# Optimization experiments

Hardware: AMD Instinct MI355X
Metric: run time of the kernel (lower is better)

Reference implementation:

```python
import jax, jax.numpy as jnp
import numpy as np

# GPT-2 small structural constants (hardcoded in the original module)
L, H, D, DH, F, V, P, S, NC = 12, 12, 768, 64, 3072, 50257, 1024, 128, 29

def _ln(x, g, b, eps=1e-5):
    m = x.mean(-1, keepdims=True)
    v = ((x - m) ** 2).mean(-1, keepdims=True)
    return (x - m) * jax.lax.rsqrt(v + eps) * g + b

def _split_w(W):  # [D, D] -> [H, D, DH]: torch _split_heads on the last (output) dim
    return jnp.transpose(W.reshape(D, H, DH), (1, 0, 2))

def _attn_heads(xln, Wqh, Wkh, Wvh, Woh, qb, kb, vb, mask):
    # xln: [H, S, D] per-head circuit inputs. Computes the weight-product attention
    # branch: (xln@Wq+bq)(xln@Wk+bk)^T scores (algebraically identical to the four
    # W_mhqk bias-expanded terms in the source), causal softmax, then
    # attn @ ((xln@Wv+bv) @ W_mho) which equals attn@Output_mhov + attn@bv_Wo.
    q = jnp.einsum('hse,hed->hsd', xln, Wqh) + qb[:, None, :]
    k = jnp.einsum('hse,hed->hsd', xln, Wkh) + kb[:, None, :]
    v = jnp.einsum('hse,hed->hsd', xln, Wvh) + vb[:, None, :]
    s = jnp.einsum('hsd,htd->hst', q, k) / (DH ** 0.5)
    s = jnp.where(mask, s, jnp.finfo(s.dtype).min)
    a = jax.nn.softmax(s, axis=-1)
    ctx = jnp.einsum('hst,htd->hsd', a, v)
    return jnp.einsum('hsd,hdf->hsf', ctx, Woh)  # [H, S, D]

def _check1(x, r, records):
    # check_representation: subtract refined-matrix-gated recorded circuit tensors
    # from layers 0..i-1 (rows >= i of records are still zero, so full contraction
    # equals contracting records[0:i+1]).
    return x - jnp.einsum('lc,lcsd->sd', r, records)

def _checkH(x, rh, records):  # batched over the 12 per-head checks
    return x[None] - jnp.einsum('hlc,lcsd->hsd', rh, records)

def _forward(input_ids, refined_matrix, wte, wpe, qkv_w, qkv_b, proj_w, proj_b,
             ln1_g, ln1_b, ln2_g, ln2_b, fc_w, fc_b, mproj_w, mproj_b, lnf_g, lnf_b):
    rm = refined_matrix.astype(wte.dtype)                 # [L*NC, L, NC]
    h = wte[input_ids[0]] + wpe[:S]                       # [S, D]
    records = jnp.zeros((L, NC, S, D), dtype=h.dtype)     # record_circuit_tensor_all
    mask = jnp.tril(jnp.ones((S, S), dtype=bool))
    gelu = lambda x: jax.nn.gelu(x, approximate=True)     # GPT-2 gelu_new
    for i in range(L):
        Wq, Wk, Wv = jnp.split(qkv_w[i], 3, axis=1)
        Wqh, Wkh, Wvh = _split_w(Wq), _split_w(Wk), _split_w(Wv)
        qb = qkv_b[i][:D].reshape(H, DH)
        kb = qkv_b[i][D:2 * D].reshape(H, DH)
        vb = qkv_b[i][2 * D:].reshape(H, DH)
        Woh = proj_w[i].reshape(H, DH, D)                 # W_mho per head
        base = i * NC
        if i > 0:
            c1 = _check1(h, rm[base], records)                       # check 0
            x2 = _checkH(h, rm[base + 1:base + 1 + H], records)      # checks 1..12
            x3 = _check1(h, rm[base + 13], records)                  # check 13
            x4 = _checkH(h, rm[base + 14:base + 14 + H], records)    # checks 14..25
        else:
            c1, x3 = h, h
            x2 = jnp.broadcast_to(h, (H, S, D))
            x4 = x2
        # circuit 2: per-head attention via weight products
        x2ln = _ln(x2, ln1_g[i], ln1_b[i])
        head2 = _attn_heads(x2ln, Wqh, Wkh, Wvh, Woh, qb, kb, vb, mask)
        c2 = head2.sum(0)
        residual = c1 + c2 + proj_b[i]                    # + W_obias
        # full MLP stream on the residual (with c_fc bias, no c_proj bias)
        stream = gelu(_ln(residual, ln2_g[i], ln2_b[i]) @ fc_w[i] + fc_b[i]) @ mproj_w[i]
        # circuit 3: bias-free MLP of the (double-LN'd) checked layer input
        x3ln = _ln(_ln(x3, ln1_g[i], ln1_b[i]), ln2_g[i], ln2_b[i])
        c3 = gelu(x3ln @ fc_w[i]) @ mproj_w[i]
        # circuit 4: per-head attention branch -> MLP composition
        x4ln = _ln(x4, ln1_g[i], ln1_b[i])
        head4 = _attn_heads(x4ln, Wqh, Wkh, Wvh, Woh, qb, kb, vb, mask)
        c4_heads = gelu(_ln(head4, ln2_g[i], ln2_b[i]) @ fc_w[i]) @ mproj_w[i]
        c5 = stream - c3 - c4_heads.sum(0)                # nonlinearity compensation
        c6 = jnp.broadcast_to(mproj_b[i], (S, D))
        ob = jnp.broadcast_to(proj_b[i], (S, D))
        rec = jnp.concatenate([c1[None], head2, c3[None], c4_heads,
                               c5[None], c6[None], ob[None]], axis=0)  # [29, S, D]
        records = records.at[i].set(rec)
        h = residual + stream + mproj_b[i]
    return _ln(h, lnf_g, lnf_b) @ wte.T                   # logits [S, V]

def setup_inputs():
    key = jax.random.key(0)
    ks = jax.random.split(key, 16)
    sd = 0.02
    n = lambda k, shp: (jax.random.normal(k, shp) * sd).astype(jnp.float32)
    return {
        'input_ids': jax.random.randint(ks[0], (1, S), 0, V),
        'label_ids': jax.random.randint(ks[1], (1, S), 0, V),
        'refined_matrix': jax.random.randint(ks[2], (L * NC, L, NC), 0, 2).astype(jnp.int32),
        'wte': n(ks[3], (V, D)),
        'wpe': n(ks[4], (P, D)),
        'qkv_w': n(ks[5], (L, D, 3 * D)),
        'qkv_b': n(ks[6], (L, 3 * D)),
        'proj_w': n(ks[7], (L, D, D)),
        'proj_b': n(ks[8], (L, D)),
        'ln1_g': jnp.ones((L, D), jnp.float32),
        'ln1_b': jnp.zeros((L, D), jnp.float32),
        'ln2_g': jnp.ones((L, D), jnp.float32),
        'ln2_b': jnp.zeros((L, D), jnp.float32),
        'fc_w': n(ks[9], (L, D, F)),
        'fc_b': n(ks[10], (L, F)),
        'mproj_w': n(ks[11], (L, F, D)),
        'mproj_b': n(ks[12], (L, D)),
        'lnf_g': jnp.ones((D,), jnp.float32),
        'lnf_b': jnp.zeros((D,), jnp.float32),
    }

def reference(input_ids, label_ids, refined_matrix, wte, wpe, qkv_w, qkv_b, proj_w, proj_b,
              ln1_g, ln1_b, ln2_g, ln2_b, fc_w, fc_b, mproj_w, mproj_b, lnf_g, lnf_b):
    return _forward(input_ids, refined_matrix, wte, wpe, qkv_w, qkv_b, proj_w, proj_b,
                    ln1_g, ln1_b, ln2_g, ln2_b, fc_w, fc_b, mproj_w, mproj_b, lnf_g, lnf_b)
```

## Files before the change

kernel.cpp:

```cpp
#include <hip/hip_runtime.h>

#define SS 128
#define DD 768
#define HH 12
#define DHD 64
#define FF 3072
#define VV 50257
#define NCC 29
#define LL 12
#define SD (SS*DD)
#define SF (SS*FF)
#define TMAX (LL*NCC)

typedef unsigned short u16;
typedef __attribute__((ext_vector_type(8))) short short8;
typedef __attribute__((ext_vector_type(4))) float f32x4;

__device__ inline u16 f2bf(float f) {
    union { float f; unsigned u; } x; x.f = f;
    unsigned r = x.u + 0x7fffu + ((x.u >> 16) & 1u);
    return (u16)(r >> 16);
}

__global__ void k_masku(const int* __restrict__ rm, unsigned* __restrict__ lmu) {
    int idx = blockIdx.x * 256 + threadIdx.x;
    if (idx >= LL * TMAX) return;
    int i = idx / TMAX, t = idx % TMAX;
    unsigned m = 0;
    for (int j = 0; j < 26; j++)
        m |= (unsigned)(rm[(size_t)(i * NCC + j) * TMAX + t] & 1) << j;
    lmu[idx] = m;
}

__global__ void k_embed(const int* __restrict__ ids, const float* __restrict__ wte,
                        const float* __restrict__ wpe, float* __restrict__ h) {
    int sd = blockIdx.x * 256 + threadIdx.x;
    if (sd >= SD) return;
    int s = sd / DD, d = sd % DD;
    h[sd] = wte[(size_t)ids[s] * DD + d] + wpe[sd];
}

__global__ void k_cvt(const float* __restrict__ in, u16* __restrict__ out, int n4) {
    int i = blockIdx.x * 256 + threadIdx.x;
    if (i >= n4) return;
    float4 v = *(const float4*)(in + (size_t)i * 4);
    u16* o = out + (size_t)i * 4;
    o[0] = f2bf(v.x); o[1] = f2bf(v.y); o[2] = f2bf(v.z); o[3] = f2bf(v.w);
}

__global__ void k_qkvb(const float* __restrict__ qkv_b, float* __restrict__ qkvbp) {
    int idx = blockIdx.x * 256 + threadIdx.x;
    if (idx >= LL * 3 * DD) return;
    int l = idx / (3 * DD), r = idx % (3 * DD);
    int p = r / DD, rem = r % DD, h = rem / DHD, j = rem % DHD;
    qkvbp[(size_t)l * 3 * DD + h * 192 + p * DHD + j] = qkv_b[idx];
}

__global__ __launch_bounds__(256) void k_wt(const float* __restrict__ W, u16* __restrict__ WT,
                                            int K, int N, int remap,
                                            long long sW, long long sWT) {
    __shared__ float T[64][65];
    const float* Wb = W + (size_t)blockIdx.z * sW;
    u16* WTb = WT + (size_t)blockIdx.z * sWT;
    int n0 = blockIdx.x * 64, k0 = blockIdx.y * 64;
    int c = threadIdx.x & 63, r0 = threadIdx.x >> 6;
#pragma unroll
    for (int i = 0; i < 16; i++) {
        int r = r0 + 4 * i;
        T[r][c] = Wb[(size_t)(k0 + r) * N + n0 + c];
    }
    __syncthreads();
    int ob = n0 >> 6;
    if (remap) { int p = ob / 12, h = ob % 12; ob = h * 3 + p; }
    size_t orow0 = (size_t)ob * 64;
#pragma unroll
    for (int i = 0; i < 16; i++) {
        int a = r0 + 4 * i;
        WTb[(orow0 + a) * K + k0 + c] = f2bf(T[c][a]);
    }
}

__global__ __launch_bounds__(256) void k_check(
    const float* __restrict__ records, const unsigned* __restrict__ lmu,
    const float* __restrict__ h, float* __restrict__ rec0, float* __restrict__ x24,
    float* __restrict__ x3, int layer) {
    __shared__ float red[4][26][128];
    int lane = threadIdx.x & 63, w = threadIdx.x >> 6;
    int sd0 = blockIdx.x * 128;
    int sd = sd0 + lane * 2;
    int T = layer * NCC;
    int Tq = (T + 3) >> 2;
    int tb = w * Tq, te = tb + Tq; if (te > T) te = T;
    float2 acc[26];
#pragma unroll
    for (int j = 0; j < 26; j++) { acc[j].x = 0.f; acc[j].y = 0.f; }
    const unsigned* lm = lmu + layer * TMAX;
    const float* rp = records + sd;
    int t = tb;
    for (; t + 8 <= te; t += 8) {
        float2 r[8];
        unsigned mv[8];
#pragma unroll
        for (int u = 0; u < 8; u++) r[u] = *(const float2*)(rp + (size_t)(t + u) * SD);
#pragma unroll
        for (int u = 0; u < 8; u++) mv[u] = lm[t + u];
#pragma unroll
        for (int u = 0; u < 8; u++) {
            unsigned m = __builtin_amdgcn_readfirstlane(mv[u]);
#pragma unroll
            for (int j = 0; j < 26; j++) {
                float mm = (m & (1u << j)) ? 1.0f : 0.0f;
                acc[j].x = fmaf(mm, r[u].x, acc[j].x);
                acc[j].y = fmaf(mm, r[u].y, acc[j].y);
            }
        }
    }
    for (; t < te; t++) {
        float2 r = *(const float2*)(rp + (size_t)t * SD);
        unsigned m = __builtin_amdgcn_readfirstlane(lm[t]);
#pragma unroll
        for (int j = 0; j < 26; j++) {
            float mm = (m & (1u << j)) ? 1.0f : 0.0f;
            acc[j].x = fmaf(mm, r.x, acc[j].x);
            acc[j].y = fmaf(mm, r.y, acc[j].y);
        }
    }
#pragma unroll
    for (int j = 0; j < 26; j++)
        *(float2*)&red[w][j][lane * 2] = acc[j];
    __syncthreads();
    for (int o = threadIdx.x; o < 26 * 128; o += 256) {
        int j = o >> 7, sdl = o & 127;
        float s = red[0][j][sdl] + red[1][j][sdl] + red[2][j][sdl] + red[3][j][sdl];
        float v = h[sd0 + sdl] - s;
        float* dst;
        if (j == 0) dst = rec0;
        else if (j <= 12) dst = x24 + (size_t)(j - 1) * SD;
        else if (j == 13) dst = x3;
        else dst = x24 + (size_t)(12 + j - 14) * SD;
        dst[sd0 + sdl] = v;
    }
}

__device__ inline void wave_ln(float (&vals)[12], int lane, const float* __restrict__ g,
                               const float* __restrict__ b) {
    float s = 0.f;
#pragma unroll
    for (int i = 0; i < 12; i++) s += vals[i];
#pragma unroll
    for (int m = 32; m >= 1; m >>= 1) s += __shfl_xor(s, m, 64);
    float mean = s * (1.f / DD);
    float vs = 0.f;
#pragma unroll
    for (int i = 0; i < 12; i++) { float d = vals[i] - mean; vs += d * d; }
#pragma unroll
    for (int m = 32; m >= 1; m >>= 1) vs += __shfl_xor(vs, m, 64);
    float rstd = rsqrtf(vs * (1.f / DD) + 1e-5f);
#pragma unroll
    for (int i = 0; i < 12; i++)
        vals[i] = (vals[i] - mean) * rstd * g[lane + 64 * i] + b[lane + 64 * i];
}

__global__ __launch_bounds__(256) void k_ln(const float* __restrict__ in, float* __restrict__ outf,
                                            u16* __restrict__ outb,
                                            const float* __restrict__ g, const float* __restrict__ b,
                                            int R) {
    int row = blockIdx.x * 4 + (threadIdx.x >> 6);
    if (row >= R) return;
    int lane = threadIdx.x & 63;
    const float* x = in + (size_t)row * DD;
    float vals[12];
#pragma unroll
    for (int i = 0; i < 12; i++) vals[i] = x[lane + 64 * i];
    wave_ln(vals, lane, g, b);
#pragma unroll
    for (int i = 0; i < 12; i++) {
        int d = lane + 64 * i;
        if (outf) outf[(size_t)row * DD + d] = vals[i];
        if (outb) outb[(size_t)row * DD + d] = f2bf(vals[i]);
    }
}

__global__ __launch_bounds__(256) void k_rln(const float* __restrict__ reci,
                                             const float* __restrict__ x3,
                                             const float* __restrict__ tmp4,
                                             const float* __restrict__ proj_b_i,
                                             float* __restrict__ resid,
                                             u16* __restrict__ mlpAb,
                                             const float* __restrict__ l1g, const float* __restrict__ l1b,
                                             const float* __restrict__ l2g, const float* __restrict__ l2b) {
    int rowid = blockIdx.x * 4 + (threadIdx.x >> 6);
    int z = rowid >> 7, s = rowid & 127;
    int lane = threadIdx.x & 63;
    float vals[12];
    if (z == 0) {
        const float* src = x3 + (size_t)s * DD;
#pragma unroll
        for (int i = 0; i < 12; i++) vals[i] = src[lane + 64 * i];
        wave_ln(vals, lane, l1g, l1b);
    } else if (z <= 12) {
        const float* src = tmp4 + (size_t)(z - 1) * SD + (size_t)s * DD;
#pragma unroll
        for (int i = 0; i < 12; i++) vals[i] = src[lane + 64 * i];
    } else {
        const float* base = reci + (size_t)s * DD;
#pragma unroll
        for (int i = 0; i < 12; i++) {
            int d = lane + 64 * i;
            float a = base[d];
#pragma unroll
            for (int j = 1; j <= 12; j++) a += base[(size_t)j * SD + d];
            a += proj_b_i[d];
            vals[i] = a;
            resid[(size_t)s * DD + d] = a;
        }
    }
    wave_ln(vals, lane, l2g, l2b);
    u16* o = mlpAb + (size_t)z * SD + (size_t)s * DD;
#pragma unroll
    for (int i = 0; i < 12; i++) o[lane + 64 * i] = f2bf(vals[i]);
}

__global__ __launch_bounds__(256) void k_mm(
    const u16* __restrict__ A, const u16* __restrict__ BT,
    const float* __restrict__ bias, void* __restrict__ Cv, void* __restrict__ Cv2,
    int N, int K, int lda, int ldbt, int ldc,
    long long sA, long long sBT, long long sC, long long sBias,
    int zMod, int zHi, int biasLo, int mode) {
    __shared__ u16 As[128][40];
    __shared__ u16 Bs[64][40];
    int z = blockIdx.z;
    int zb = z % zMod;
    const u16* Ab = A + (size_t)z * sA;
    const u16* Bb = BT + (size_t)zb * sBT;
    int n0 = blockIdx.x * 64;
    int nSplit = gridDim.y;
    int kLen = K / nSplit;
    int kOff = blockIdx.y * kLen;
    int kEnd = kOff + kLen;
    int tid = threadIdx.x;
    int lane = tid & 63, wid = tid >> 6;
    int wm = (wid >> 1) * 64, wn = (wid & 1) * 32;
    int l15 = lane & 15, l4 = lane >> 4;
    int sr = tid >> 2, sseg = tid & 3;
    int bn = n0 + sr;
    f32x4 acc[4][2];
#pragma unroll
    for (int i = 0; i < 4; i++) { acc[i][0] = (f32x4)0.f; acc[i][1] = (f32x4)0.f; }
    uint4 zero; zero.x = 0u; zero.y = 0u; zero.z = 0u; zero.w = 0u;
    uint4 a0 = *(const uint4*)(Ab + (size_t)sr * lda + kOff + sseg * 8);
    uint4 a1 = *(const uint4*)(Ab + (size_t)(sr + 64) * lda + kOff + sseg * 8);
    uint4 bv = (bn < N) ? *(const uint4*)(Bb + (size_t)bn * ldbt + kOff + sseg * 8) : zero;
    for (int k0 = kOff; k0 < kEnd; k0 += 32) {
        __syncthreads();
        *(uint4*)&As[sr][sseg * 8] = a0;
        *(uint4*)&As[sr + 64][sseg * 8] = a1;
        *(uint4*)&Bs[sr][sseg * 8] = bv;
        __syncthreads();
        if (k0 + 32 < kEnd) {
            a0 = *(const uint4*)(Ab + (size_t)sr * lda + k0 + 32 + sseg * 8);
            a1 = *(const uint4*)(Ab + (size_t)(sr + 64) * lda + k0 + 32 + sseg * 8);
            bv = (bn < N) ? *(const uint4*)(Bb + (size_t)bn * ldbt + k0 + 32 + sseg * 8) : zero;
        }
        short8 af[4], bfr[2];
#pragma unroll
        for (int i = 0; i < 4; i++) af[i] = *(const short8*)&As[wm + i * 16 + l15][l4 * 8];
#pragma unroll
        for (int j = 0; j < 2; j++) bfr[j] = *(const short8*)&Bs[wn + j * 16 + l15][l4 * 8];
#pragma unroll
        for (int i = 0; i < 4; i++)
#pragma unroll
            for (int j = 0; j < 2; j++)
                acc[i][j] = __builtin_amdgcn_mfma_f32_16x16x32_bf16(af[i], bfr[j], acc[i][j], 0, 0, 0);
    }
    const float* bp = (bias != nullptr && z >= biasLo) ? bias + (size_t)zb * sBias : nullptr;
    void* Cuse;
    int zc;
    if (nSplit > 1) { Cuse = Cv; zc = z * nSplit + blockIdx.y; }
    else { Cuse = (z >= zHi) ? Cv2 : Cv; zc = (z >= zHi) ? z - zHi : z; }
    if (mode == 0) {
        float* Cb = (float*)Cuse + (size_t)zc * sC;
#pragma unroll
        for (int i = 0; i < 4; i++) {
            int row = wm + i * 16 + l4 * 4;
#pragma unroll
            for (int j = 0; j < 2; j++) {
                int col = n0 + wn + j * 16 + l15;
                if (col >= N) continue;
                float bb = bp ? bp[col] : 0.f;
#pragma unroll
                for (int r = 0; r < 4; r++)
                    Cb[(size_t)(row + r) * ldc + col] = acc[i][j][r] + bb;
            }
        }
    } else {
        u16* Cb = (u16*)Cuse + (size_t)zc * sC;
#pragma unroll
        for (int i = 0; i < 4; i++) {
            int row = wm + i * 16 + l4 * 4;
#pragma unroll
            for (int j = 0; j < 2; j++) {
                int col = n0 + wn + j * 16 + l15;
                if (col >= N) continue;
                float bb = bp ? bp[col] : 0.f;
#pragma unroll
                for (int r = 0; r < 4; r++) {
                    float v = acc[i][j][r] + bb;
                    float c = v + 0.044715f * v * v * v;
                    float gv = 0.5f * v * (1.f + tanhf(0.7978845608028654f * c));
                    Cb[(size_t)(row + r) * ldc + col] = f2bf(gv);
                }
            }
        }
    }
}

__global__ __launch_bounds__(256) void k_attn(const float* __restrict__ qkvp,
                                              const float* __restrict__ qbias,
                                              u16* __restrict__ ctx) {
    __shared__ float kv[SS * DHD];
    __shared__ float qs[16][DHD];
    __shared__ float sc[16][130];
    int z = blockIdx.y, s0 = blockIdx.x * 16;
    const float* p0 = qkvp + (size_t)z * 4 * (SS * 192);
    const float* p1 = p0 + SS * 192;
    const float* p2 = p1 + SS * 192;
    const float* p3 = p2 + SS * 192;
    const float* qb = qbias + (size_t)(z % 12) * 192;
    int tid = threadIdx.x;
    for (int idx = tid; idx < SS * DHD; idx += 256) {
        int t = idx >> 6, d = idx & 63;
        int o = t * 192 + 64 + d;
        kv[idx] = p0[o] + p1[o] + p2[o] + p3[o] + qb[64 + d];
    }
    for (int idx = tid; idx < 16 * DHD; idx += 256) {
        int r = idx >> 6, d = idx & 63;
        int o = (s0 + r) * 192 + d;
        qs[r][d] = p0[o] + p1[o] + p2[o] + p3[o] + qb[d];
    }
    __syncthreads();
    int r = tid >> 4, tt = tid & 15;
    int s = s0 + r;
    float pl[8];
#pragma unroll
    for (int u = 0; u < 8; u++) {
        int t = tt + 16 * u;
        float dot;
        if (t <= s) {
            dot = 0.f;
            for (int d = 0; d < DHD; d++) dot += qs[r][d] * kv[t * DHD + d];
            dot *= 0.125f;
        } else {
            dot = -1e30f;
        }
        pl[u] = dot;
    }
    float mx = pl[0];
#pragma unroll
    for (int u = 1; u < 8; u++) mx = fmaxf(mx, pl[u]);
#pragma unroll
    for (int m = 1; m < 16; m <<= 1) mx = fmaxf(mx, __shfl_xor(mx, m, 16));
    float sum = 0.f;
#pragma unroll
    for (int u = 0; u < 8; u++) { pl[u] = __expf(pl[u] - mx); sum += pl[u]; }
#pragma unroll
    for (int m = 1; m < 16; m <<= 1) sum += __shfl_xor(sum, m, 16);
    float inv = 1.f / sum;
#pragma unroll
    for (int u = 0; u < 8; u++) sc[r][tt + 16 * u] = pl[u] * inv;
    __syncthreads();
    for (int idx = tid; idx < SS * DHD; idx += 256) {
        int t = idx >> 6, d = idx & 63;
        int o = t * 192 + 128 + d;
        kv[idx] = p0[o] + p1[o] + p2[o] + p3[o] + qb[128 + d];
    }
    __syncthreads();
    int d = tid & 63, r0 = tid >> 6;
#pragma unroll
    for (int u = 0; u < 4; u++) {
        int rr = r0 + 4 * u;
        float a = 0.f;
        for (int t = 0; t < SS; t++) a += sc[rr][t] * kv[t * DHD + d];
        ctx[(size_t)z * SS * DHD + (size_t)(s0 + rr) * DHD + d] = f2bf(a);
    }
}

__global__ void k_red(const float* __restrict__ part, const float* __restrict__ resid,
                      const float* __restrict__ proj_b_i, const float* __restrict__ mproj_b_i,
                      float* __restrict__ reci, float* __restrict__ h) {
    int sd = blockIdx.x * 256 + threadIdx.x;
    if (sd >= SD) return;
    int d = sd % DD;
    float v0 = 0.f, s4 = 0.f, st = 0.f;
#pragma unroll
    for (int zz = 0; zz < 14; zz++) {
        const float* p = part + (size_t)zz * 4 * SD + sd;
        float v = p[0] + p[SD] + p[2 * SD] + p[3 * SD];
        if (zz == 0) { v0 = v; reci[(size_t)13 * SD + sd] = v; }
        else if (zz <= 12) { s4 += v; reci[(size_t)(13 + zz) * SD + sd] = v; }
        else st = v;
    }
    reci[(size_t)26 * SD + sd] = st - v0 - s4;
    reci[(size_t)27 * SD + sd] = mproj_b_i[d];
    reci[(size_t)28 * SD + sd] = proj_b_i[d];
    h[sd] = resid[sd] + st + mproj_b_i[d];
}

extern "C" void kernel_launch(void* const* d_in, const int* in_sizes, int n_in,
                              void* d_out, int out_size, void* d_ws, size_t ws_size,
                              hipStream_t stream) {
    const int* ids = (const int*)d_in[0];
    const int* rm = (const int*)d_in[2];
    const float* wte = (const float*)d_in[3];
    const float* wpe = (const float*)d_in[4];
    const float* qkv_w = (const float*)d_in[5];
    const float* qkv_b = (const float*)d_in[6];
    const float* proj_w = (const float*)d_in[7];
    const float* proj_b = (const float*)d_in[8];
    const float* ln1_g = (const float*)d_in[9];
    const float* ln1_b = (const float*)d_in[10];
    const float* ln2_g = (const float*)d_in[11];
    const float* ln2_b = (const float*)d_in[12];
    const float* fc_w = (const float*)d_in[13];
    const float* fc_b = (const float*)d_in[14];
    const float* mproj_w = (const float*)d_in[15];
    const float* mproj_b = (const float*)d_in[16];
    const float* lnf_g = (const float*)d_in[17];
    const float* lnf_b = (const float*)d_in[18];
    float* out = (float*)d_out;

    float* ws = (float*)d_ws;
    size_t off = 0;
    float* records = ws + off; off += (size_t)LL * NCC * SD;
    float* x24  = ws + off; off += (size_t)24 * SD;
    float* tmp4 = ws + off; off += (size_t)12 * SD;
    float* h    = ws + off; off += SD;
    float* x3   = ws + off; off += SD;
    float* resid= ws + off; off += SD;
    float* qkvp = ws + off; off += (size_t)24 * 4 * SS * 192;
    float* mpp  = ws + off; off += (size_t)14 * 4 * SD;
    float* qkvbp= ws + off; off += (size_t)LL * 3 * DD;
    u16* xlnb  = (u16*)(ws + off); off += (size_t)24 * SD / 2;
    u16* mlpAb = (u16*)(ws + off); off += (size_t)14 * SD / 2;
    u16* hfcb  = (u16*)(ws + off); off += (size_t)14 * SF / 2;
    u16* ctxb  = (u16*)(ws + off); off += (size_t)24 * SS * DHD / 2;
    u16* lnfb  = (u16*)(ws + off); off += SD / 2;
    u16* qkvhT = (u16*)(ws + off); off += (size_t)LL * 2304 * DD / 2;
    u16* fcT   = (u16*)(ws + off); off += (size_t)LL * FF * DD / 2;
    u16* mprojT= (u16*)(ws + off); off += (size_t)LL * DD * FF / 2;
    u16* projT = (u16*)(ws + off); off += (size_t)LL * DD * DD / 2;
    u16* wteb  = (u16*)(ws + off); off += (size_t)VV * DD / 2;
    unsigned* lmu = (unsigned*)(ws + off);

    k_masku<<<(LL * TMAX + 255) / 256, 256, 0, stream>>>(rm, lmu);
    k_embed<<<SD / 256, 256, 0, stream>>>(ids, wte, wpe, h);
    k_cvt<<<((VV * DD / 4) + 255) / 256, 256, 0, stream>>>(wte, wteb, VV * DD / 4);
    k_qkvb<<<(LL * 3 * DD + 255) / 256, 256, 0, stream>>>(qkv_b, qkvbp);
    k_wt<<<dim3(36, 12, 12), 256, 0, stream>>>(qkv_w, qkvhT, DD, 3 * DD, 1,
                                               (long long)DD * 3 * DD, (long long)2304 * DD);
    k_wt<<<dim3(48, 12, 12), 256, 0, stream>>>(fc_w, fcT, DD, FF, 0,
                                               (long long)DD * FF, (long long)FF * DD);
    k_wt<<<dim3(12, 48, 12), 256, 0, stream>>>(mproj_w, mprojT, FF, DD, 0,
                                               (long long)FF * DD, (long long)DD * FF);
    k_wt<<<dim3(12, 12, 12), 256, 0, stream>>>(proj_w, projT, DD, DD, 0,
                                               (long long)DD * DD, (long long)DD * DD);

    for (int i = 0; i < LL; i++) {
        float* reci = records + (size_t)i * NCC * SD;
        const float* l1g = ln1_g + i * DD; const float* l1b = ln1_b + i * DD;
        const float* l2g = ln2_g + i * DD; const float* l2b = ln2_b + i * DD;
        const u16* qkvhTi = qkvhT + (size_t)i * 2304 * DD;
        const u16* fcTi = fcT + (size_t)i * FF * DD;
        const u16* mprojTi = mprojT + (size_t)i * DD * FF;
        const u16* projTi = projT + (size_t)i * DD * DD;

        k_check<<<SD / 128, 256, 0, stream>>>(records, lmu, h, reci, x24, x3, i);

        k_ln<<<24 * SS / 4, 256, 0, stream>>>(x24, nullptr, xlnb, l1g, l1b, 24 * SS);
        k_mm<<<dim3(3, 4, 24), 256, 0, stream>>>(
            xlnb, qkvhTi, nullptr, qkvp, nullptr,
            192, DD, DD, DD, 192, SD, (long long)192 * DD, (long long)SS * 192, 0, 12, 9999, 99, 0);
        k_attn<<<dim3(SS / 16, 24), 256, 0, stream>>>(qkvp, qkvbp + (size_t)i * 3 * DD, ctxb);
        k_mm<<<dim3(12, 1, 24), 256, 0, stream>>>(
            ctxb, projTi, nullptr, reci + SD, tmp4,
            DD, DHD, DHD, DD, DD, (long long)SS * DHD, 64, SD, 0, 12, 12, 99, 0);
        k_rln<<<14 * SS / 4, 256, 0, stream>>>(reci, x3, tmp4, proj_b + i * DD, resid, mlpAb,
                                               l1g, l1b, l2g, l2b);
        k_mm<<<dim3(48, 1, 14), 256, 0, stream>>>(
            mlpAb, fcTi, fc_b + (size_t)i * FF, hfcb, nullptr,
            FF, DD, DD, DD, FF, SD, 0, SF, 0, 1, 9999, 13, 1);
        k_mm<<<dim3(12, 4, 14), 256, 0, stream>>>(
            hfcb, mprojTi, nullptr, mpp, nullptr,
            DD, FF, FF, FF, DD, SF, 0, SD, 0, 1, 9999, 99, 0);
        k_red<<<SD / 256, 256, 0, stream>>>(mpp, resid, proj_b + i * DD, mproj_b + i * DD,
                                            reci, h);
    }

    k_ln<<<SS / 4, 256, 0, stream>>>(h, nullptr, lnfb, lnf_g, lnf_b, SS);
    k_mm<<<dim3((VV + 63) / 64, 1, 1), 256, 0, stream>>>(
        lnfb, wteb, nullptr, out, nullptr,
        VV, DD, DD, DD, VV, 0, 0, 0, 0, 1, 9999, 99, 0);
}
```

Baseline: 1.821 ms.

## Fuse attention with output projection and fold MLP reduction into next check

The attention kernel now keeps the context in shared memory and multiplies it directly by the per-head slice of the projection weights with MFMA. This removes the bf16 context round trip and one GEMM launch per layer. The k_red reduction of MLP partials is folded into the next layer's k_check, which rebuilds h and the last 16 record slots in shared memory and uses them straight from registers instead of re-reading them from global. This cuts two launches per layer and some traffic, at the cost of extra serial work in a wave of k_check and redundant projT reads across attention blocks.

```diff
diff --git a/kernel.cpp b/kernel.cpp
--- a/kernel.cpp
+++ b/kernel.cpp
@@ -83,14 +83,53 @@
 __global__ __launch_bounds__(256) void k_check(
     const float* __restrict__ records, const unsigned* __restrict__ lmu,
     const float* __restrict__ h, float* __restrict__ rec0, float* __restrict__ x24,
-    float* __restrict__ x3, int layer) {
+    float* __restrict__ x3, int layer,
+    const float* __restrict__ mpp, const float* __restrict__ resid,
+    const float* __restrict__ proj_b_p, const float* __restrict__ mproj_b_p,
+    float* __restrict__ recprev) {
     __shared__ float red[4][26][128];
+    __shared__ float vred[14][128];
+    __shared__ float hloc[128];
     int lane = threadIdx.x & 63, w = threadIdx.x >> 6;
     int sd0 = blockIdx.x * 128;
+    int d0 = sd0 % DD;
+    int T = layer * NCC;
+    if (layer > 0) {
+        for (int idx = threadIdx.x; idx < 14 * 128; idx += 256) {
+            int z = idx >> 7, sdl = idx & 127;
+            const float* p = mpp + (size_t)z * 4 * SD + sd0 + sdl;
+            vred[z][sdl] = p[0] + p[SD] + p[2 * SD] + p[3 * SD];
+        }
+        __syncthreads();
+        if (threadIdx.x < 128) {
+            int sdl = threadIdx.x;
+            int sd = sd0 + sdl, d = d0 + sdl;
+            float v0 = vred[0][sdl];
+            float st = vred[13][sdl];
+            float s4 = 0.f;
+#pragma unroll
+            for (int z = 1; z <= 12; z++) s4 += vred[z][sdl];
+            float c5 = st - v0 - s4;
+            float mb = mproj_b_p[d], pb = proj_b_p[d];
+            float hn = resid[sd] + st + mb;
+            hloc[sdl] = hn;
+            recprev[(size_t)13 * SD + sd] = v0;
+#pragma unroll
+            for (int z = 1; z <= 12; z++) recprev[(size_t)(13 + z) * SD + sd] = vred[z][sdl];
+            recprev[(size_t)26 * SD + sd] = c5;
+            recprev[(size_t)27 * SD + sd] = mb;
+            recprev[(size_t)28 * SD + sd] = pb;
+            vred[13][sdl] = c5;
+        }
+        __syncthreads();
+    } else {
+        if (threadIdx.x < 128) hloc[threadIdx.x] = h[sd0 + threadIdx.x];
+        __syncthreads();
+    }
     int sd = sd0 + lane * 2;
-    int T = layer * NCC;
-    int Tq = (T + 3) >> 2;
-    int tb = w * Tq, te = tb + Tq; if (te > T) te = T;
+    int Tm = (layer > 0) ? T - 16 : 0;
+    int Tq = (Tm + 3) >> 2;
+    int tb = w * Tq, te = tb + Tq; if (te > Tm) te = Tm;
     float2 acc[26];
 #pragma unroll
     for (int j = 0; j < 26; j++) { acc[j].x = 0.f; acc[j].y = 0.f; }
@@ -125,6 +164,22 @@
             acc[j].y = fmaf(mm, r.y, acc[j].y);
         }
     }
+    if (layer > 0 && w == 3) {
+#pragma unroll
+        for (int c = 13; c <= 28; c++) {
+            unsigned m = __builtin_amdgcn_readfirstlane(lm[Tm + c - 13]);
+            float rx, ry;
+            if (c <= 26) { rx = vred[c - 13][lane * 2]; ry = vred[c - 13][lane * 2 + 1]; }
+            else if (c == 27) { rx = mproj_b_p[d0 + lane * 2]; ry = mproj_b_p[d0 + lane * 2 + 1]; }
+            else { rx = proj_b_p[d0 + lane * 2]; ry = proj_b_p[d0 + lane * 2 + 1]; }
+#pragma unroll
+            for (int j = 0; j < 26; j++) {
+                float mm = (m & (1u << j)) ? 1.0f : 0.0f;
+                acc[j].x = fmaf(mm, rx, acc[j].x);
+                acc[j].y = fmaf(mm, ry, acc[j].y);
+            }
+        }
+    }
 #pragma unroll
     for (int j = 0; j < 26; j++)
         *(float2*)&red[w][j][lane * 2] = acc[j];
@@ -132,7 +187,7 @@
     for (int o = threadIdx.x; o < 26 * 128; o += 256) {
         int j = o >> 7, sdl = o & 127;
         float s = red[0][j][sdl] + red[1][j][sdl] + red[2][j][sdl] + red[3][j][sdl];
-        float v = h[sd0 + sdl] - s;
+        float v = hloc[sdl] - s;
         float* dst;
         if (j == 0) dst = rec0;
         else if (j <= 12) dst = x24 + (size_t)(j - 1) * SD;
@@ -315,18 +370,22 @@
     }
 }
 
-__global__ __launch_bounds__(256) void k_attn(const float* __restrict__ qkvp,
-                                              const float* __restrict__ qbias,
-                                              u16* __restrict__ ctx) {
+__global__ __launch_bounds__(256) void k_attnp(const float* __restrict__ qkvp,
+                                               const float* __restrict__ qbias,
+                                               const u16* __restrict__ projT,
+                                               float* __restrict__ outLo,
+                                               float* __restrict__ outHi) {
     __shared__ float kv[SS * DHD];
     __shared__ float qs[16][DHD];
     __shared__ float sc[16][130];
+    __shared__ u16 cxs[16][72];
     int z = blockIdx.y, s0 = blockIdx.x * 16;
+    int hb = z % 12;
     const float* p0 = qkvp + (size_t)z * 4 * (SS * 192);
     const float* p1 = p0 + SS * 192;
     const float* p2 = p1 + SS * 192;
     const float* p3 = p2 + SS * 192;
-    const float* qb = qbias + (size_t)(z % 12) * 192;
+    const float* qb = qbias + (size_t)hb * 192;
     int tid = threadIdx.x;
     for (int idx = tid; idx < SS * DHD; idx += 256) {
         int t = idx >> 6, d = idx & 63;
@@ -381,28 +440,37 @@
         int rr = r0 + 4 * u;
         float a = 0.f;
         for (int t = 0; t < SS; t++) a += sc[rr][t] * kv[t * DHD + d];
-        ctx[(size_t)z * SS * DHD + (size_t)(s0 + rr) * DHD + d] = f2bf(a);
-    }
-}
-
-__global__ void k_red(const float* __restrict__ part, const float* __restrict__ resid,
-                      const float* __restrict__ proj_b_i, const float* __restrict__ mproj_b_i,
-                      float* __restrict__ reci, float* __restrict__ h) {
+        cxs[rr][d] = f2bf(a);
+    }
+    __syncthreads();
+    int lane = tid & 63, w = tid >> 6;
+    int l15 = lane & 15, l4 = lane >> 4;
+    short8 af[2];
+#pragma unroll
+    for (int ks = 0; ks < 2; ks++) af[ks] = *(const short8*)&cxs[l15][ks * 32 + l4 * 8];
+    float* ob = (z < 12) ? outLo + (size_t)z * SD : outHi + (size_t)(z - 12) * SD;
+#pragma unroll
+    for (int nt = 0; nt < 12; nt++) {
+        int n0t = (w * 12 + nt) * 16;
+        f32x4 acc = (f32x4)0.f;
+#pragma unroll
+        for (int ks = 0; ks < 2; ks++) {
+            short8 bf = *(const short8*)(projT + (size_t)(n0t + l15) * DD + hb * DHD + ks * 32 + l4 * 8);
+            acc = __builtin_amdgcn_mfma_f32_16x16x32_bf16(af[ks], bf, acc, 0, 0, 0);
+        }
+#pragma unroll
+        for (int rr = 0; rr < 4; rr++)
+            ob[(size_t)(s0 + l4 * 4 + rr) * DD + n0t + l15] = acc[rr];
+    }
+}
+
+__global__ void k_hfin(const float* __restrict__ mpp, const float* __restrict__ resid,
+                       const float* __restrict__ mproj_b_i, float* __restrict__ h) {
     int sd = blockIdx.x * 256 + threadIdx.x;
     if (sd >= SD) return;
     int d = sd % DD;
-    float v0 = 0.f, s4 = 0.f, st = 0.f;
-#pragma unroll
-    for (int zz = 0; zz < 14; zz++) {
-        const float* p = part + (size_t)zz * 4 * SD + sd;
-        float v = p[0] + p[SD] + p[2 * SD] + p[3 * SD];
-        if (zz == 0) { v0 = v; reci[(size_t)13 * SD + sd] = v; }
-        else if (zz <= 12) { s4 += v; reci[(size_t)(13 + zz) * SD + sd] = v; }
-        else st = v;
-    }
-    reci[(size_t)26 * SD + sd] = st - v0 - s4;
-    reci[(size_t)27 * SD + sd] = mproj_b_i[d];
-    reci[(size_t)28 * SD + sd] = proj_b_i[d];
+    const float* p = mpp + (size_t)13 * 4 * SD + sd;
+    float st = p[0] + p[SD] + p[2 * SD] + p[3 * SD];
     h[sd] = resid[sd] + st + mproj_b_i[d];
 }
 
@@ -443,7 +511,6 @@
     u16* xlnb  = (u16*)(ws + off); off += (size_t)24 * SD / 2;
     u16* mlpAb = (u16*)(ws + off); off += (size_t)14 * SD / 2;
     u16* hfcb  = (u16*)(ws + off); off += (size_t)14 * SF / 2;
-    u16* ctxb  = (u16*)(ws + off); off += (size_t)24 * SS * DHD / 2;
     u16* lnfb  = (u16*)(ws + off); off += SD / 2;
     u16* qkvhT = (u16*)(ws + off); off += (size_t)LL * 2304 * DD / 2;
     u16* fcT   = (u16*)(ws + off); off += (size_t)LL * FF * DD / 2;
@@ -467,6 +534,9 @@
 
     for (int i = 0; i < LL; i++) {
         float* reci = records + (size_t)i * NCC * SD;
+        float* recprev = records + (size_t)(i > 0 ? i - 1 : 0) * NCC * SD;
+        const float* pbp = proj_b + (size_t)(i > 0 ? i - 1 : 0) * DD;
+        const float* mbp = mproj_b + (size_t)(i > 0 ? i - 1 : 0) * DD;
         const float* l1g = ln1_g + i * DD; const float* l1b = ln1_b + i * DD;
         const float* l2g = ln2_g + i * DD; const float* l2b = ln2_b + i * DD;
         const u16* qkvhTi = qkvhT + (size_t)i * 2304 * DD;
@@ -474,16 +544,15 @@
         const u16* mprojTi = mprojT + (size_t)i * DD * FF;
         const u16* projTi = projT + (size_t)i * DD * DD;
 
-        k_check<<<SD / 128, 256, 0, stream>>>(records, lmu, h, reci, x24, x3, i);
+        k_check<<<SD / 128, 256, 0, stream>>>(records, lmu, h, reci, x24, x3, i,
+                                              mpp, resid, pbp, mbp, recprev);
 
         k_ln<<<24 * SS / 4, 256, 0, stream>>>(x24, nullptr, xlnb, l1g, l1b, 24 * SS);
         k_mm<<<dim3(3, 4, 24), 256, 0, stream>>>(
             xlnb, qkvhTi, nullptr, qkvp, nullptr,
             192, DD, DD, DD, 192, SD, (long long)192 * DD, (long long)SS * 192, 0, 12, 9999, 99, 0);
-        k_attn<<<dim3(SS / 16, 24), 256, 0, stream>>>(qkvp, qkvbp + (size_t)i * 3 * DD, ctxb);
-        k_mm<<<dim3(12, 1, 24), 256, 0, stream>>>(
-            ctxb, projTi, nullptr, reci + SD, tmp4,
-            DD, DHD, DHD, DD, DD, (long long)SS * DHD, 64, SD, 0, 12, 12, 99, 0);
+        k_attnp<<<dim3(SS / 16, 24), 256, 0, stream>>>(qkvp, qkvbp + (size_t)i * 3 * DD,
+                                                       projTi, reci + SD, tmp4);
         k_rln<<<14 * SS / 4, 256, 0, stream>>>(reci, x3, tmp4, proj_b + i * DD, resid, mlpAb,
                                                l1g, l1b, l2g, l2b);
         k_mm<<<dim3(48, 1, 14), 256, 0, stream>>>(
@@ -492,10 +561,9 @@
         k_mm<<<dim3(12, 4, 14), 256, 0, stream>>>(
             hfcb, mprojTi, nullptr, mpp, nullptr,
             DD, FF, FF, FF, DD, SF, 0, SD, 0, 1, 9999, 99, 0);
-        k_red<<<SD / 256, 256, 0, stream>>>(mpp, resid, proj_b + i * DD, mproj_b + i * DD,
-                                            reci, h);
-    }
-
+    }
+
+    k_hfin<<<SD / 256, 256, 0, stream>>>(mpp, resid, mproj_b + (size_t)11 * DD, h);
     k_ln<<<SS / 4, 256, 0, stream>>>(h, nullptr, lnfb, lnf_g, lnf_b, SS);
     k_mm<<<dim3((VV + 63) / 64, 1, 1), 256, 0, stream>>>(
         lnfb, wteb, nullptr, out, nullptr,
```

New measurement: 2.111 ms. 15.9% more time.
